# Kernel optimization log

Measured on AMD Instinct MI355X. Metric: run time of the kernel, lower is better.

Reference implementation:

```python
import jax, jax.numpy as jnp
import numpy as np

B, NLB, NPB, SDIM = 128, 32, 160, 256  # complexes, ligand atoms, pocket CAs, scalar dim


def _uniform(key, shape, fan_in):
    # kaiming_uniform_(a=sqrt(5)) -> U(-1/sqrt(fan_in), 1/sqrt(fan_in))
    bound = 1.0 / np.sqrt(fan_in)
    return jax.random.uniform(key, shape, jnp.float32, -bound, bound)


def setup_inputs() -> dict:
    key = jax.random.key(0)
    k1, k2, k3, k4, k5 = jax.random.split(key, 5)
    NL, NP = B * NLB, B * NPB
    # block-diagonal cross adjacency: every ligand atom paired with every pocket CA
    # of the same complex (same as (batch_ligand[:,None]==batch_pocket[None,:]).nonzero().T)
    l = np.repeat(np.arange(NL, dtype=np.int32), NPB)
    p = (np.arange(B, dtype=np.int32)[:, None, None] * NPB
         + np.zeros((1, NLB, 1), dtype=np.int32)
         + np.arange(NPB, dtype=np.int32)[None, None, :]).reshape(-1)
    return {
        "s_ligand": jax.random.normal(k1, (NL, SDIM), jnp.float32),
        "s_pocket": jax.random.normal(k2, (NP, SDIM), jnp.float32),
        "l": jnp.asarray(l),
        "p": jnp.asarray(p),
        "W1": _uniform(k3, (SDIM // 2, SDIM), SDIM),
        "b1": jnp.zeros((SDIM // 2,), jnp.float32),
        "W2": _uniform(k4, (SDIM // 4, SDIM // 2), SDIM // 2),
        "b2": jnp.zeros((SDIM // 4,), jnp.float32),
        "W3": _uniform(k5, (1, SDIM // 4), SDIM // 4),
        "b3": jnp.zeros((1,), jnp.float32),
    }


def reference(s_ligand, s_pocket, l, p, W1, b1, W2, b2, W3, b3):
    # gather cross-pair embeddings and sum: s[e] = s_ligand[l[e]] + s_pocket[p[e]]
    s = s_ligand[l] + s_pocket[p]                      # [E, sdim]
    h = jax.nn.silu(s @ W1.T + b1)                     # [E, sdim/2]
    h = jax.nn.silu(h @ W2.T + b2)                     # [E, sdim/4]
    out = jax.nn.relu(h @ W3.T + b3)                   # [E, 1]
    return out.squeeze(-1)                             # [E]
```

## Files before the change

kernel.cpp:

```cpp
#include <hip/hip_runtime.h>
#include <hip/hip_bf16.h>


#define B_CPLX   128
#define NLB      32
#define NPB      160
#define SDIM     256
#define H1DIM    128
#define NL_TOT   (B_CPLX * NLB)
#define NP_TOT   (B_CPLX * NPB)
#define NROWS    (NL_TOT + NP_TOT)
#define E_TOT    (B_CPLX * NLB * NPB)

#define W1_LDS_STRIDE 264
#define JT_CHUNK 16
#define ZP_STRIDE 132

#define EDGE_BLOCKS (B_CPLX * 10)

#define NEG_LOG2E -1.4426950408889634f
#define NEG_LN2   -0.69314718055994531f

typedef __bf16 bf16x8 __attribute__((ext_vector_type(8)));
typedef __bf16 bf16x2 __attribute__((ext_vector_type(2)));
typedef unsigned short ushortx8 __attribute__((ext_vector_type(8)));
typedef unsigned short ushortx4 __attribute__((ext_vector_type(4)));
typedef unsigned uintx4 __attribute__((ext_vector_type(4)));
typedef float f32x4 __attribute__((ext_vector_type(4)));
typedef float f32x2 __attribute__((ext_vector_type(2)));

#if __has_builtin(__builtin_amdgcn_exp2f)
#define EXP2F(x) __builtin_amdgcn_exp2f(x)
#else
#define EXP2F(x) exp2f(x)
#endif

__device__ __forceinline__ unsigned short f2bf(float f) {
    unsigned u = __builtin_bit_cast(unsigned, f);
    u += 0x7FFFu + ((u >> 16) & 1u);
    return (unsigned short)(u >> 16);
}

__device__ __forceinline__ unsigned perm_hi16u(unsigned u0, unsigned u1) {
    return __builtin_amdgcn_perm(u1, u0, 0x07060302u);
}

__device__ __forceinline__ unsigned pack2_rhu(float x0, float x1) {
    unsigned u0 = __builtin_bit_cast(unsigned, x0) + 0x8000u;
    unsigned u1 = __builtin_bit_cast(unsigned, x1) + 0x8000u;
    return perm_hi16u(u0, u1);
}

__device__ __forceinline__ bf16x8 pack8_rne(const float* x) {
    bf16x8 r;
#pragma unroll
    for (int j = 0; j < 4; ++j) {
        f32x2 p = {x[2 * j], x[2 * j + 1]};
        bf16x2 b = __builtin_convertvector(p, bf16x2);
        r[2 * j]     = b[0];
        r[2 * j + 1] = b[1];
    }
    return r;
}

__device__ __forceinline__ void pack_split(const float* x, bf16x8& hi, bf16x8& lo) {
    uintx4 h, l;
#pragma unroll
    for (int j = 0; j < 4; ++j) {
        float x0 = x[2 * j], x1 = x[2 * j + 1];
        unsigned u0 = __builtin_bit_cast(unsigned, x0);
        unsigned u1 = __builtin_bit_cast(unsigned, x1);
        h[j] = perm_hi16u(u0, u1);
        float hf0 = __builtin_bit_cast(float, u0 & 0xFFFF0000u);
        float hf1 = __builtin_bit_cast(float, u1 & 0xFFFF0000u);
        l[j] = pack2_rhu(x0 - hf0, x1 - hf1);
    }
    hi = __builtin_bit_cast(bf16x8, h);
    lo = __builtin_bit_cast(bf16x8, l);
}

__device__ __forceinline__ float silu_u(float t) {
    float e = EXP2F(t);
    float r = __builtin_amdgcn_rcpf(1.0f + e);
    return t * r;
}

__global__ __launch_bounds__(256) void proj_kernel(
    const float* __restrict__ s_lig, const float* __restrict__ s_poc,
    const float* __restrict__ W1,    const float* __restrict__ b1,
    const float* __restrict__ W2,
    float* __restrict__ Z,           unsigned short* __restrict__ W2F)
{
    __shared__ unsigned short w1s[64 * W1_LDS_STRIDE];

    const int tid  = threadIdx.x;
    const int tg   = blockIdx.x >> 1;
    const int half = blockIdx.x & 1;

    if (blockIdx.x == 0) {
#pragma unroll
        for (int s = 0; s < 4; ++s) {
            const int slot   = tid + s * 256;
            const int lane_s = slot & 63;
            const int chunk  = slot >> 6;
            const int nt     = chunk >> 2;
            const int ks     = chunk & 3;
            const int n      = nt * 16 + (lane_s & 15);
            const int k0     = ks * 32 + (lane_s >> 4) * 8;
            const float* wsrc = W2 + (size_t)n * H1DIM + k0;
            f32x4 wa = *(const f32x4*)wsrc;
            f32x4 wb = *(const f32x4*)(wsrc + 4);
            ushortx8 us;
#pragma unroll
            for (int j = 0; j < 4; ++j) {
                us[j]     = f2bf(wa[j]);
                us[4 + j] = f2bf(wb[j]);
            }
            *(ushortx8*)(&W2F[slot * 8]) = us;
        }
    }

    {
        const f32x4* w4 = (const f32x4*)(W1 + (size_t)half * 64 * SDIM);
#pragma unroll
        for (int r = 0; r < 2; ++r) {
            f32x4 t[8];
#pragma unroll
            for (int s = 0; s < 8; ++s) t[s] = w4[tid + (r * 8 + s) * 256];
#pragma unroll
            for (int s = 0; s < 8; ++s) {
                const int u = tid + (r * 8 + s) * 256;
                const int n = u >> 6;
                const int k4 = u & 63;
                ushortx4 us;
#pragma unroll
                for (int j = 0; j < 4; ++j) us[j] = f2bf(t[s][j] * NEG_LOG2E);
                *(ushortx4*)(&w1s[n * W1_LDS_STRIDE + k4 * 4]) = us;
            }
        }
    }
    __syncthreads();

    const int lane = tid & 63;
    const int widx = tid >> 6;
    const int c    = lane & 15;
    const int q    = lane >> 4;
    const int tile = tg * 4 + widx;
    const int row  = tile * 16 + c;

    const float* src = (row < NL_TOT) ? (s_lig + (size_t)row * SDIM)
                                      : (s_poc + (size_t)(row - NL_TOT) * SDIM);

    f32x4 acc[4];
#pragma unroll
    for (int nt = 0; nt < 4; ++nt) acc[nt] = (f32x4){0.f, 0.f, 0.f, 0.f};

#pragma unroll
    for (int ks = 0; ks < 8; ++ks) {
        const int k0 = ks * 32 + q * 8;
        f32x4 xa = *reinterpret_cast<const f32x4*>(src + k0);
        f32x4 xb = *reinterpret_cast<const f32x4*>(src + k0 + 4);
        float xv[8] = {xa[0], xa[1], xa[2], xa[3], xb[0], xb[1], xb[2], xb[3]};
        bf16x8 ahi, alo;
        pack_split(xv, ahi, alo);
        bf16x8 bfrag[4];
#pragma unroll
        for (int nt = 0; nt < 4; ++nt)
            bfrag[nt] = *reinterpret_cast<const bf16x8*>(
                &w1s[(nt * 16 + c) * W1_LDS_STRIDE + k0]);
#pragma unroll
        for (int nt = 0; nt < 4; ++nt)
            acc[nt] = __builtin_amdgcn_mfma_f32_16x16x32_bf16(ahi, bfrag[nt], acc[nt], 0, 0, 0);
#pragma unroll
        for (int nt = 0; nt < 4; ++nt)
            acc[nt] = __builtin_amdgcn_mfma_f32_16x16x32_bf16(alo, bfrag[nt], acc[nt], 0, 0, 0);
    }

    const int mb = tile * 16 + q * 4;
#pragma unroll
    for (int nt = 0; nt < 4; ++nt) {
        const int n = half * 64 + nt * 16 + c;
        const float bias = b1[n] * NEG_LOG2E;
#pragma unroll
        for (int r = 0; r < 4; ++r) {
            const int m = mb + r;
            float v = acc[nt][r];
            if (m < NL_TOT) v += bias;
            Z[(size_t)m * H1DIM + n] = v;
        }
    }
}

__global__ __launch_bounds__(256) void edge_kernel(
    const float* __restrict__ Z,  const unsigned short* __restrict__ W2F,
    const float* __restrict__ b2, const float* __restrict__ W3,
    const float* __restrict__ b3, float* __restrict__ out)
{
    __shared__ float zp[JT_CHUNK * ZP_STRIDE];
    __shared__ float zl[NLB * H1DIM];
    __shared__ unsigned short w2s[16 * 64 * 8];

    const int tid = threadIdx.x;
    const int b   = blockIdx.x / 10;
    const int jt  = blockIdx.x - b * 10;

    {
#pragma unroll
        for (int s = 0; s < 4; ++s) {
            const int slot = tid + s * 256;
            *(ushortx8*)(&w2s[slot * 8]) = *(const ushortx8*)(&W2F[slot * 8]);
        }
    }

    {
        const float* zpg = Z + (size_t)(NL_TOT + b * NPB + jt * JT_CHUNK) * H1DIM;
#pragma unroll
        for (int s = 0; s < 2; ++s) {
            const int u   = tid + s * 256;
            const int row = u >> 5;
            const int c4  = u & 31;
            *(f32x4*)(&zp[row * ZP_STRIDE + c4 * 4]) =
                *(const f32x4*)(zpg + (size_t)row * H1DIM + c4 * 4);
        }
    }

    {
        const float* zlg = Z + (size_t)(b * NLB) * H1DIM;
#pragma unroll
        for (int s = 0; s < 4; ++s) {
            const int u   = tid + s * 256;
            const int row = u >> 5;
            const int c4  = u & 31;
            *(f32x4*)(&zl[row * H1DIM + c4 * 4]) =
                *(const f32x4*)(zlg + (size_t)row * H1DIM + c4 * 4);
        }
    }

    const int lane = tid & 63;
    const int widx = tid >> 6;
    const int c    = lane & 15;
    const int q    = lane >> 4;

    f32x4 b2v[4], w3v[4];
#pragma unroll
    for (int nt = 0; nt < 4; ++nt) {
        f32x4 bv = *(const f32x4*)(b2 + nt * 16 + q * 4);
        f32x4 wv = *(const f32x4*)(W3 + nt * 16 + q * 4);
        b2v[nt] = bv * NEG_LOG2E;
        w3v[nt] = wv * NEG_LN2;
    }
    const float b3v = b3[0];

    __syncthreads();

    const float* prow = &zp[c * ZP_STRIDE];
    const unsigned short* wbase = &w2s[lane * 8];

#pragma unroll
    for (int h = 0; h < 2; ++h) {
        f32x4 acc[4][4];
#pragma unroll
        for (int a = 0; a < 4; ++a)
#pragma unroll
            for (int nt = 0; nt < 4; ++nt) acc[a][nt] = b2v[nt];

        const float* lrow0 = &zl[(h * 16 + widx * 4) * H1DIM];

#pragma unroll
        for (int ks = 0; ks < 4; ++ks) {
            const int k0 = ks * 32 + q * 8;
            bf16x8 bfr[4];
#pragma unroll
            for (int nt = 0; nt < 4; ++nt)
                bfr[nt] = *(const bf16x8*)(wbase + (nt * 4 + ks) * 512);
            f32x4 pa = *(const f32x4*)(prow + k0);
            f32x4 pb = *(const f32x4*)(prow + k0 + 4);
#pragma unroll
            for (int a = 0; a < 4; ++a) {
                f32x4 la0 = *(const f32x4*)(lrow0 + a * H1DIM + k0);
                f32x4 la1 = *(const f32x4*)(lrow0 + a * H1DIM + k0 + 4);
                float hv[8];
#pragma unroll
                for (int j = 0; j < 4; ++j) {
                    hv[j]     = silu_u(pa[j] + la0[j]);
                    hv[4 + j] = silu_u(pb[j] + la1[j]);
                }
                bf16x8 af = pack8_rne(hv);
#pragma unroll
                for (int nt = 0; nt < 4; ++nt)
                    acc[a][nt] = __builtin_amdgcn_mfma_f32_16x16x32_bf16(bfr[nt], af, acc[a][nt], 0, 0, 0);
            }
        }

#pragma unroll
        for (int at = 0; at < 4; ++at) {
            const f32x4* A = acc[at];
            float s0 = 0.f, s1 = 0.f, s2 = 0.f, s3 = 0.f;
#pragma unroll
            for (int nt = 0; nt < 4; ++nt) {
                s0 += silu_u(A[nt][0]) * w3v[nt][0];
                s1 += silu_u(A[nt][1]) * w3v[nt][1];
                s2 += silu_u(A[nt][2]) * w3v[nt][2];
                s3 += silu_u(A[nt][3]) * w3v[nt][3];
            }
            float v = (s0 + s1) + (s2 + s3);
            v += __shfl_xor(v, 16);
            v += __shfl_xor(v, 32);
            if (lane < 16) {
                const int e0 = (b * NLB + h * 16 + widx * 4 + at) * NPB + jt * JT_CHUNK;
                out[e0 + lane] = fmaxf(v + b3v, 0.0f);
            }
        }
    }
}

extern "C" void kernel_launch(void* const* d_in, const int* in_sizes, int n_in,
                              void* d_out, int out_size, void* d_ws, size_t ws_size,
                              hipStream_t stream)
{
    const float* s_lig = (const float*)d_in[0];
    const float* s_poc = (const float*)d_in[1];
    const float* W1    = (const float*)d_in[4];
    const float* b1    = (const float*)d_in[5];
    const float* W2    = (const float*)d_in[6];
    const float* b2    = (const float*)d_in[7];
    const float* W3    = (const float*)d_in[8];
    const float* b3    = (const float*)d_in[9];

    float* Z = (float*)d_ws;
    unsigned short* W2F = (unsigned short*)(Z + (size_t)NROWS * H1DIM);

    hipLaunchKernelGGL(proj_kernel, dim3(NROWS / 16 / 4 * 2), dim3(256), 0, stream,
                       s_lig, s_poc, W1, b1, W2, Z, W2F);
    hipLaunchKernelGGL(edge_kernel, dim3(EDGE_BLOCKS), dim3(256), 0, stream,
                       Z, W2F, b2, W3, b3, (float*)d_out);
}
```

Before: 130.3 us.

## Double edge-kernel block to 512 threads and use hardware bf16 conversions

The edge kernel now launches 8 waves per block, so each wave handles 4 ligand rows once instead of looping over two halves, and the cooperative LDS loads are respread over 512 threads. Scalar bf16 packing (manual round-to-nearest and round-half-up) is replaced by vector convertvector-based RNE conversions in both kernels. The intent is more waves in flight to hide LDS and transcendental latency, with less serial work per wave. The larger block may cut blocks per CU if register or LDS use limits occupancy, and the bf16 low-part rounding in pack_split changes slightly.

```diff
diff --git a/kernel.cpp b/kernel.cpp
--- a/kernel.cpp
+++ b/kernel.cpp
@@ -26,6 +26,7 @@
 typedef unsigned short ushortx8 __attribute__((ext_vector_type(8)));
 typedef unsigned short ushortx4 __attribute__((ext_vector_type(4)));
 typedef unsigned uintx4 __attribute__((ext_vector_type(4)));
+typedef unsigned uintx2 __attribute__((ext_vector_type(2)));
 typedef float f32x4 __attribute__((ext_vector_type(4)));
 typedef float f32x2 __attribute__((ext_vector_type(2)));
 
@@ -35,32 +36,28 @@
 #define EXP2F(x) exp2f(x)
 #endif
 
-__device__ __forceinline__ unsigned short f2bf(float f) {
-    unsigned u = __builtin_bit_cast(unsigned, f);
-    u += 0x7FFFu + ((u >> 16) & 1u);
-    return (unsigned short)(u >> 16);
-}
-
 __device__ __forceinline__ unsigned perm_hi16u(unsigned u0, unsigned u1) {
     return __builtin_amdgcn_perm(u1, u0, 0x07060302u);
 }
 
-__device__ __forceinline__ unsigned pack2_rhu(float x0, float x1) {
-    unsigned u0 = __builtin_bit_cast(unsigned, x0) + 0x8000u;
-    unsigned u1 = __builtin_bit_cast(unsigned, x1) + 0x8000u;
-    return perm_hi16u(u0, u1);
+__device__ __forceinline__ unsigned cvt2_rne(float x0, float x1) {
+    f32x2 p = {x0, x1};
+    bf16x2 b = __builtin_convertvector(p, bf16x2);
+    return __builtin_bit_cast(unsigned, b);
+}
+
+__device__ __forceinline__ uintx2 pack4_rne_u(f32x4 v) {
+    uintx2 r;
+    r[0] = cvt2_rne(v[0], v[1]);
+    r[1] = cvt2_rne(v[2], v[3]);
+    return r;
 }
 
 __device__ __forceinline__ bf16x8 pack8_rne(const float* x) {
-    bf16x8 r;
-#pragma unroll
-    for (int j = 0; j < 4; ++j) {
-        f32x2 p = {x[2 * j], x[2 * j + 1]};
-        bf16x2 b = __builtin_convertvector(p, bf16x2);
-        r[2 * j]     = b[0];
-        r[2 * j + 1] = b[1];
-    }
-    return r;
+    uintx4 h;
+#pragma unroll
+    for (int j = 0; j < 4; ++j) h[j] = cvt2_rne(x[2 * j], x[2 * j + 1]);
+    return __builtin_bit_cast(bf16x8, h);
 }
 
 __device__ __forceinline__ void pack_split(const float* x, bf16x8& hi, bf16x8& lo) {
@@ -73,7 +70,7 @@
         h[j] = perm_hi16u(u0, u1);
         float hf0 = __builtin_bit_cast(float, u0 & 0xFFFF0000u);
         float hf1 = __builtin_bit_cast(float, u1 & 0xFFFF0000u);
-        l[j] = pack2_rhu(x0 - hf0, x1 - hf1);
+        l[j] = cvt2_rne(x0 - hf0, x1 - hf1);
     }
     hi = __builtin_bit_cast(bf16x8, h);
     lo = __builtin_bit_cast(bf16x8, l);
@@ -110,13 +107,12 @@
             const float* wsrc = W2 + (size_t)n * H1DIM + k0;
             f32x4 wa = *(const f32x4*)wsrc;
             f32x4 wb = *(const f32x4*)(wsrc + 4);
-            ushortx8 us;
-#pragma unroll
-            for (int j = 0; j < 4; ++j) {
-                us[j]     = f2bf(wa[j]);
-                us[4 + j] = f2bf(wb[j]);
-            }
-            *(ushortx8*)(&W2F[slot * 8]) = us;
+            uintx4 us;
+            us[0] = cvt2_rne(wa[0], wa[1]);
+            us[1] = cvt2_rne(wa[2], wa[3]);
+            us[2] = cvt2_rne(wb[0], wb[1]);
+            us[3] = cvt2_rne(wb[2], wb[3]);
+            *(uintx4*)(&W2F[slot * 8]) = us;
         }
     }
 
@@ -132,10 +128,8 @@
                 const int u = tid + (r * 8 + s) * 256;
                 const int n = u >> 6;
                 const int k4 = u & 63;
-                ushortx4 us;
-#pragma unroll
-                for (int j = 0; j < 4; ++j) us[j] = f2bf(t[s][j] * NEG_LOG2E);
-                *(ushortx4*)(&w1s[n * W1_LDS_STRIDE + k4 * 4]) = us;
+                uintx2 us = pack4_rne_u(t[s] * NEG_LOG2E);
+                *(uintx2*)(&w1s[n * W1_LDS_STRIDE + k4 * 4]) = us;
             }
         }
     }
@@ -191,7 +185,7 @@
     }
 }
 
-__global__ __launch_bounds__(256) void edge_kernel(
+__global__ __launch_bounds__(512) void edge_kernel(
     const float* __restrict__ Z,  const unsigned short* __restrict__ W2F,
     const float* __restrict__ b2, const float* __restrict__ W3,
     const float* __restrict__ b3, float* __restrict__ out)
@@ -206,29 +200,25 @@
 
     {
 #pragma unroll
-        for (int s = 0; s < 4; ++s) {
-            const int slot = tid + s * 256;
+        for (int s = 0; s < 2; ++s) {
+            const int slot = tid + s * 512;
             *(ushortx8*)(&w2s[slot * 8]) = *(const ushortx8*)(&W2F[slot * 8]);
         }
     }
 
     {
         const float* zpg = Z + (size_t)(NL_TOT + b * NPB + jt * JT_CHUNK) * H1DIM;
-#pragma unroll
-        for (int s = 0; s < 2; ++s) {
-            const int u   = tid + s * 256;
-            const int row = u >> 5;
-            const int c4  = u & 31;
-            *(f32x4*)(&zp[row * ZP_STRIDE + c4 * 4]) =
-                *(const f32x4*)(zpg + (size_t)row * H1DIM + c4 * 4);
-        }
+        const int row = tid >> 5;
+        const int c4  = tid & 31;
+        *(f32x4*)(&zp[row * ZP_STRIDE + c4 * 4]) =
+            *(const f32x4*)(zpg + (size_t)row * H1DIM + c4 * 4);
     }
 
     {
         const float* zlg = Z + (size_t)(b * NLB) * H1DIM;
 #pragma unroll
-        for (int s = 0; s < 4; ++s) {
-            const int u   = tid + s * 256;
+        for (int s = 0; s < 2; ++s) {
+            const int u   = tid + s * 512;
             const int row = u >> 5;
             const int c4  = u & 31;
             *(f32x4*)(&zl[row * H1DIM + c4 * 4]) =
@@ -256,60 +246,57 @@
     const float* prow = &zp[c * ZP_STRIDE];
     const unsigned short* wbase = &w2s[lane * 8];
 
-#pragma unroll
-    for (int h = 0; h < 2; ++h) {
-        f32x4 acc[4][4];
-#pragma unroll
-        for (int a = 0; a < 4; ++a)
-#pragma unroll
-            for (int nt = 0; nt < 4; ++nt) acc[a][nt] = b2v[nt];
-
-        const float* lrow0 = &zl[(h * 16 + widx * 4) * H1DIM];
-
-#pragma unroll
-        for (int ks = 0; ks < 4; ++ks) {
-            const int k0 = ks * 32 + q * 8;
-            bf16x8 bfr[4];
+    f32x4 acc[4][4];
+#pragma unroll
+    for (int a = 0; a < 4; ++a)
+#pragma unroll
+        for (int nt = 0; nt < 4; ++nt) acc[a][nt] = b2v[nt];
+
+    const float* lrow0 = &zl[(widx * 4) * H1DIM];
+
+#pragma unroll
+    for (int ks = 0; ks < 4; ++ks) {
+        const int k0 = ks * 32 + q * 8;
+        bf16x8 bfr[4];
+#pragma unroll
+        for (int nt = 0; nt < 4; ++nt)
+            bfr[nt] = *(const bf16x8*)(wbase + (nt * 4 + ks) * 512);
+        f32x4 pa = *(const f32x4*)(prow + k0);
+        f32x4 pb = *(const f32x4*)(prow + k0 + 4);
+#pragma unroll
+        for (int a = 0; a < 4; ++a) {
+            f32x4 la0 = *(const f32x4*)(lrow0 + a * H1DIM + k0);
+            f32x4 la1 = *(const f32x4*)(lrow0 + a * H1DIM + k0 + 4);
+            float hv[8];
+#pragma unroll
+            for (int j = 0; j < 4; ++j) {
+                hv[j]     = silu_u(pa[j] + la0[j]);
+                hv[4 + j] = silu_u(pb[j] + la1[j]);
+            }
+            bf16x8 af = pack8_rne(hv);
 #pragma unroll
             for (int nt = 0; nt < 4; ++nt)
-                bfr[nt] = *(const bf16x8*)(wbase + (nt * 4 + ks) * 512);
-            f32x4 pa = *(const f32x4*)(prow + k0);
-            f32x4 pb = *(const f32x4*)(prow + k0 + 4);
-#pragma unroll
-            for (int a = 0; a < 4; ++a) {
-                f32x4 la0 = *(const f32x4*)(lrow0 + a * H1DIM + k0);
-                f32x4 la1 = *(const f32x4*)(lrow0 + a * H1DIM + k0 + 4);
-                float hv[8];
-#pragma unroll
-                for (int j = 0; j < 4; ++j) {
-                    hv[j]     = silu_u(pa[j] + la0[j]);
-                    hv[4 + j] = silu_u(pb[j] + la1[j]);
-                }
-                bf16x8 af = pack8_rne(hv);
-#pragma unroll
-                for (int nt = 0; nt < 4; ++nt)
-                    acc[a][nt] = __builtin_amdgcn_mfma_f32_16x16x32_bf16(bfr[nt], af, acc[a][nt], 0, 0, 0);
-            }
-        }
-
-#pragma unroll
-        for (int at = 0; at < 4; ++at) {
-            const f32x4* A = acc[at];
-            float s0 = 0.f, s1 = 0.f, s2 = 0.f, s3 = 0.f;
-#pragma unroll
-            for (int nt = 0; nt < 4; ++nt) {
-                s0 += silu_u(A[nt][0]) * w3v[nt][0];
-                s1 += silu_u(A[nt][1]) * w3v[nt][1];
-                s2 += silu_u(A[nt][2]) * w3v[nt][2];
-                s3 += silu_u(A[nt][3]) * w3v[nt][3];
-            }
-            float v = (s0 + s1) + (s2 + s3);
-            v += __shfl_xor(v, 16);
-            v += __shfl_xor(v, 32);
-            if (lane < 16) {
-                const int e0 = (b * NLB + h * 16 + widx * 4 + at) * NPB + jt * JT_CHUNK;
-                out[e0 + lane] = fmaxf(v + b3v, 0.0f);
-            }
+                acc[a][nt] = __builtin_amdgcn_mfma_f32_16x16x32_bf16(bfr[nt], af, acc[a][nt], 0, 0, 0);
+        }
+    }
+
+#pragma unroll
+    for (int at = 0; at < 4; ++at) {
+        const f32x4* A = acc[at];
+        float s0 = 0.f, s1 = 0.f, s2 = 0.f, s3 = 0.f;
+#pragma unroll
+        for (int nt = 0; nt < 4; ++nt) {
+            s0 += silu_u(A[nt][0]) * w3v[nt][0];
+            s1 += silu_u(A[nt][1]) * w3v[nt][1];
+            s2 += silu_u(A[nt][2]) * w3v[nt][2];
+            s3 += silu_u(A[nt][3]) * w3v[nt][3];
+        }
+        float v = (s0 + s1) + (s2 + s3);
+        v += __shfl_xor(v, 16);
+        v += __shfl_xor(v, 32);
+        if (lane < 16) {
+            const int e0 = (b * NLB + widx * 4 + at) * NPB + jt * JT_CHUNK;
+            out[e0 + lane] = fmaxf(v + b3v, 0.0f);
         }
     }
 }
@@ -332,6 +319,6 @@
 
     hipLaunchKernelGGL(proj_kernel, dim3(NROWS / 16 / 4 * 2), dim3(256), 0, stream,
                        s_lig, s_poc, W1, b1, W2, Z, W2F);
-    hipLaunchKernelGGL(edge_kernel, dim3(EDGE_BLOCKS), dim3(256), 0, stream,
+    hipLaunchKernelGGL(edge_kernel, dim3(EDGE_BLOCKS), dim3(512), 0, stream,
                        Z, W2F, b2, W3, b3, (float*)d_out);
 }
```

Result: faster. 126.4 us (-3.0%).
